# Kernel tuning notes

Hardware: AMD Instinct MI355X
Metric: run time of the kernel (lower is better)

The kernel has to match this reference:

```python
import jax, jax.numpy as jnp
import numpy as np

B, S, H = 32, 1024, 512  # batch, src_len, hidden_dim


def setup_inputs() -> dict:
    key = jax.random.key(0)
    k1, k2, k3, k4, k5 = jax.random.split(key, 5)
    hidden = jax.random.normal(k1, (B, H), dtype=jnp.float32)
    encoder_outputs = jax.random.normal(k2, (B, S, 2 * H), dtype=jnp.float32)
    # nn.Linear(3H, H): weight stored here as [3H, H] (input-major) with bias [H]
    W = jax.random.normal(k3, (3 * H, H), dtype=jnp.float32) / np.sqrt(3 * H)
    b = jax.random.normal(k4, (H,), dtype=jnp.float32) * 0.01
    v = jax.random.normal(k5, (H,), dtype=jnp.float32) / np.sqrt(H)
    return {"hidden": hidden, "encoder_outputs": encoder_outputs, "W": W, "b": b, "v": v}


def reference(hidden, encoder_outputs, W, b, v):
    # concat((repeat(hidden), encoder_outputs)) @ W  ==  hidden @ W[:H] (broadcast) + enc @ W[H:]
    Wh, We = W[:H], W[H:]                         # [H,H], [2H,H]
    h_proj = hidden @ Wh                           # [B,H]
    e_proj = jnp.einsum('bse,eh->bsh', encoder_outputs, We)  # [B,S,H]
    energy = jnp.tanh(h_proj[:, None, :] + e_proj + b)       # [B,S,H]
    # bmm(v[B,1,H], energy^T[B,H,S]) -> scores [B,S]
    scores = jnp.einsum('bsh,h->bs', energy, v)
    return jax.nn.softmax(scores, axis=1)
```

## Files before the change

kernel.cpp:

```cpp
#include <hip/hip_runtime.h>
#include <math.h>

#define B_ 32
#define S_ 1024
#define H_ 512
#define K_ 1024
#define M_ (B_ * S_)

typedef __attribute__((ext_vector_type(8))) short bf16x8;
typedef __attribute__((ext_vector_type(16))) float f32x16;

__device__ __forceinline__ void split_bf16(float f, unsigned short& hi, unsigned short& lo) {
    unsigned u = __float_as_uint(f);
    unsigned r = u + 0x8000u;
    hi = (unsigned short)(r >> 16);
    float fh = __uint_as_float(r & 0xffff0000u);
    float res = f - fh;
    lo = (unsigned short)((__float_as_uint(res) + 0x8000u) >> 16);
}

__device__ __forceinline__ void split8_store(const float4& x, const float4& y,
                                             unsigned short* hiP, unsigned short* loP) {
    float f[8] = {x.x, x.y, x.z, x.w, y.x, y.y, y.z, y.w};
    unsigned hr[8], lr[8];
    #pragma unroll
    for (int i = 0; i < 8; ++i) {
        unsigned u = __float_as_uint(f[i]);
        unsigned r = u + 0x8000u;
        hr[i] = r;
        float fh = __uint_as_float(r & 0xffff0000u);
        lr[i] = __float_as_uint(f[i] - fh) + 0x8000u;
    }
    uint4 Hv, Lv;
    Hv.x = __builtin_amdgcn_perm(hr[1], hr[0], 0x07060302u);
    Hv.y = __builtin_amdgcn_perm(hr[3], hr[2], 0x07060302u);
    Hv.z = __builtin_amdgcn_perm(hr[5], hr[4], 0x07060302u);
    Hv.w = __builtin_amdgcn_perm(hr[7], hr[6], 0x07060302u);
    Lv.x = __builtin_amdgcn_perm(lr[1], lr[0], 0x07060302u);
    Lv.y = __builtin_amdgcn_perm(lr[3], lr[2], 0x07060302u);
    Lv.z = __builtin_amdgcn_perm(lr[5], lr[4], 0x07060302u);
    Lv.w = __builtin_amdgcn_perm(lr[7], lr[6], 0x07060302u);
    *reinterpret_cast<uint4*>(hiP) = Hv;
    *reinterpret_cast<uint4*>(loP) = Lv;
}

__device__ __forceinline__ float fast_tanh(float x) {
    float xc = fminf(fmaxf(x, -15.f), 15.f);
    float t = __expf(2.0f * xc);
    return (t - 1.0f) * __builtin_amdgcn_rcpf(t + 1.0f);
}

__device__ __forceinline__ void async_copy16(const void* g, void* l) {
    __builtin_amdgcn_global_load_lds(
        (const __attribute__((address_space(1))) void*)g,
        (__attribute__((address_space(3))) void*)l, 16, 0, 0);
}

__global__ __launch_bounds__(256) void prep_kernel(
    const float* __restrict__ hidden, const float* __restrict__ W,
    const float* __restrict__ bias, float* __restrict__ hb,
    unsigned short* __restrict__ Wh, unsigned short* __restrict__ Wl)
{
    __shared__ float red[4][64];
    __shared__ float t[32][33];
    const int bx = blockIdx.x;
    if (bx < 256) {
        const int tid = threadIdx.x;
        const int h0  = (bx & 7) * 64;
        const int b   = bx >> 3;
        const int h   = h0 + (tid & 63);
        const int ks  = tid >> 6;
        const float* hrow = hidden + b * H_;
        float acc = 0.f;
        #pragma unroll 8
        for (int k = ks * 128; k < ks * 128 + 128; ++k)
            acc = fmaf(hrow[k], W[(size_t)k * H_ + h], acc);
        red[ks][tid & 63] = acc;
        __syncthreads();
        if (tid < 64)
            hb[b * H_ + h0 + tid] = red[0][tid] + red[1][tid] + red[2][tid]
                                  + red[3][tid] + bias[h0 + tid];
    } else {
        const float* We = W + (size_t)H_ * H_;
        const int cx = bx - 256;
        const int k0 = (cx & 31) * 32, n0 = (cx >> 5) * 32;
        const int tx = threadIdx.x & 31, ty = threadIdx.x >> 5;
        #pragma unroll
        for (int j = 0; j < 4; ++j) {
            const int k = ty + 8 * j;
            t[k][tx] = We[(size_t)(k0 + k) * H_ + n0 + tx];
        }
        __syncthreads();
        #pragma unroll
        for (int j = 0; j < 4; ++j) {
            const int n = ty + 8 * j;
            unsigned short hi, lo;
            split_bf16(t[tx][n], hi, lo);
            Wh[(size_t)(n0 + n) * K_ + k0 + tx] = hi;
            Wl[(size_t)(n0 + n) * K_ + k0 + tx] = lo;
        }
    }
}

__global__ __launch_bounds__(256, 2) void gemm_fused(
    const float* __restrict__ EO,
    const unsigned short* __restrict__ Bth,
    const unsigned short* __restrict__ Btl,
    const float* __restrict__ hb, const float* __restrict__ v,
    float* __restrict__ partial)
{
    __shared__ unsigned short ldsA[2][2][4096];
    __shared__ unsigned short ldsB[2][2][4096];

    const int tid  = threadIdx.x;
    const int bid  = blockIdx.x;
    const int j    = bid >> 3;
    const int mt   = (bid & 7) * 32 + (j >> 2);
    const int nt   = j & 3;
    const int row0 = mt * 128;
    const int col0 = nt * 128;
    const int batch = row0 >> 10;

    const int lane   = tid & 63;
    const int wave   = tid >> 6;
    const int wm     = wave >> 1, wn = wave & 1;
    const int lane32 = lane & 31, khalf = lane >> 5;

    size_t gaA[2];
    int offA[2];
    #pragma unroll
    for (int s = 0; s < 2; ++s) {
        const int seg = tid + 256 * s;
        const int m = seg >> 2, sg = seg & 3;
        gaA[s] = (size_t)(row0 + m) * K_ + sg * 8;
        offA[s] = m * 32 + (sg ^ ((m >> 1) & 3)) * 8;
    }
    size_t gb[2];
    int offB[2];
    #pragma unroll
    for (int jj = 0; jj < 2; ++jj) {
        const int iss = wave * 2 + jj;
        const int r   = iss * 16 + (lane >> 2);
        const int qg  = (lane & 3) ^ ((r >> 1) & 3);
        gb[jj] = (size_t)(col0 + r) * K_ + qg * 8;
        offB[jj] = iss * 512;
    }

    f32x16 acc[2][2];
    #pragma unroll
    for (int fi = 0; fi < 2; ++fi)
        #pragma unroll
        for (int fj = 0; fj < 2; ++fj)
            #pragma unroll
            for (int e = 0; e < 16; ++e)
                acc[fi][fj][e] = 0.f;

    float4 a0[2], a1[2];
    #pragma unroll
    for (int s = 0; s < 2; ++s) {
        a0[s] = *reinterpret_cast<const float4*>(EO + gaA[s]);
        a1[s] = *reinterpret_cast<const float4*>(EO + gaA[s] + 4);
    }
    #pragma unroll
    for (int jj = 0; jj < 2; ++jj) {
        async_copy16(Bth + gb[jj], &ldsB[0][0][offB[jj]]);
        async_copy16(Btl + gb[jj], &ldsB[0][1][offB[jj]]);
    }
    #pragma unroll
    for (int s = 0; s < 2; ++s)
        split8_store(a0[s], a1[s], &ldsA[0][0][offA[s]], &ldsA[0][1][offA[s]]);

    for (int i = 0; i < 32; ++i) {
        __syncthreads();
        const int cur = i & 1, nxt = cur ^ 1;
        const int k0n = 32 * (i + 1);
        if (i < 31) {
            #pragma unroll
            for (int s = 0; s < 2; ++s) {
                a0[s] = *reinterpret_cast<const float4*>(EO + gaA[s] + k0n);
                a1[s] = *reinterpret_cast<const float4*>(EO + gaA[s] + k0n + 4);
            }
            #pragma unroll
            for (int jj = 0; jj < 2; ++jj) {
                async_copy16(Bth + gb[jj] + k0n, &ldsB[nxt][0][offB[jj]]);
                async_copy16(Btl + gb[jj] + k0n, &ldsB[nxt][1][offB[jj]]);
            }
        }

        bf16x8 a_h[2][2], a_l[2][2], b_h[2][2], b_l[2][2];
        #pragma unroll
        for (int fi = 0; fi < 2; ++fi) {
            const int m   = wm * 64 + fi * 32 + lane32;
            const int swz = (m >> 1) & 3;
            #pragma unroll
            for (int ks = 0; ks < 2; ++ks) {
                const int sa = (ks * 2 + khalf) ^ swz;
                a_h[fi][ks] = *reinterpret_cast<const bf16x8*>(&ldsA[cur][0][m * 32 + sa * 8]);
                a_l[fi][ks] = *reinterpret_cast<const bf16x8*>(&ldsA[cur][1][m * 32 + sa * 8]);
            }
        }
        #pragma unroll
        for (int fj = 0; fj < 2; ++fj) {
            const int n   = wn * 64 + fj * 32 + lane32;
            const int swz = (n >> 1) & 3;
            #pragma unroll
            for (int ks = 0; ks < 2; ++ks) {
                const int sb = (ks * 2 + khalf) ^ swz;
                b_h[fj][ks] = *reinterpret_cast<const bf16x8*>(&ldsB[cur][0][n * 32 + sb * 8]);
                b_l[fj][ks] = *reinterpret_cast<const bf16x8*>(&ldsB[cur][1][n * 32 + sb * 8]);
            }
        }
        #pragma unroll
        for (int fi = 0; fi < 2; ++fi)
            #pragma unroll
            for (int fj = 0; fj < 2; ++fj)
                #pragma unroll
                for (int ks = 0; ks < 2; ++ks) {
                    acc[fi][fj] = __builtin_amdgcn_mfma_f32_32x32x16_bf16(
                        a_h[fi][ks], b_h[fj][ks], acc[fi][fj], 0, 0, 0);
                    acc[fi][fj] = __builtin_amdgcn_mfma_f32_32x32x16_bf16(
                        a_h[fi][ks], b_l[fj][ks], acc[fi][fj], 0, 0, 0);
                    acc[fi][fj] = __builtin_amdgcn_mfma_f32_32x32x16_bf16(
                        a_l[fi][ks], b_h[fj][ks], acc[fi][fj], 0, 0, 0);
                }

        if (i < 31) {
            #pragma unroll
            for (int s = 0; s < 2; ++s)
                split8_store(a0[s], a1[s],
                             &ldsA[nxt][0][offA[s]], &ldsA[nxt][1][offA[s]]);
        }
    }

    const float* hb_row = hb + batch * H_;
    float hbv[2], vv[2];
    #pragma unroll
    for (int fj = 0; fj < 2; ++fj) {
        const int c = col0 + wn * 64 + fj * 32 + lane32;
        hbv[fj] = hb_row[c];
        vv[fj]  = v[c];
    }
    float* red = reinterpret_cast<float*>(&ldsA[0][0][0]);
    #pragma unroll
    for (int fi = 0; fi < 2; ++fi)
        #pragma unroll
        for (int r = 0; r < 16; ++r) {
            float rs = 0.f;
            #pragma unroll
            for (int fj = 0; fj < 2; ++fj)
                rs = fmaf(fast_tanh(acc[fi][fj][r] + hbv[fj]), vv[fj], rs);
            rs += __shfl_xor(rs, 1, 64);
            rs += __shfl_xor(rs, 2, 64);
            rs += __shfl_xor(rs, 4, 64);
            rs += __shfl_xor(rs, 8, 64);
            rs += __shfl_xor(rs, 16, 64);
            if (lane32 == 0) {
                const int row = wm * 64 + fi * 32 + (r & 3) + 8 * (r >> 2) + 4 * khalf;
                red[row * 2 + wn] = rs;
            }
        }
    __syncthreads();
    if (tid < 128)
        partial[(size_t)nt * M_ + row0 + tid] = red[tid * 2] + red[tid * 2 + 1];
}

__global__ __launch_bounds__(256) void softmax_kernel(
    const float* __restrict__ partial, float* __restrict__ out)
{
    const int b = blockIdx.x;
    const int tid = threadIdx.x;
    float val[4];
    float lmax = -3.0e38f;
    #pragma unroll
    for (int q = 0; q < 4; ++q) {
        const int idx = b * S_ + tid + 256 * q;
        float sum = partial[idx] + partial[M_ + idx] + partial[2 * M_ + idx] +
                    partial[3 * M_ + idx];
        val[q] = sum;
        lmax = fmaxf(lmax, sum);
    }
    #pragma unroll
    for (int off = 32; off > 0; off >>= 1)
        lmax = fmaxf(lmax, __shfl_down(lmax, off, 64));
    __shared__ float wmax[4];
    if ((tid & 63) == 0) wmax[tid >> 6] = lmax;
    __syncthreads();
    const float gmax = fmaxf(fmaxf(wmax[0], wmax[1]), fmaxf(wmax[2], wmax[3]));
    float lsum = 0.0f;
    #pragma unroll
    for (int q = 0; q < 4; ++q) {
        val[q] = expf(val[q] - gmax);
        lsum += val[q];
    }
    #pragma unroll
    for (int off = 32; off > 0; off >>= 1)
        lsum += __shfl_down(lsum, off, 64);
    __shared__ float wsum[4];
    if ((tid & 63) == 0) wsum[tid >> 6] = lsum;
    __syncthreads();
    const float inv = 1.0f / (wsum[0] + wsum[1] + wsum[2] + wsum[3]);
    #pragma unroll
    for (int q = 0; q < 4; ++q)
        out[b * S_ + tid + 256 * q] = val[q] * inv;
}

extern "C" void kernel_launch(void* const* d_in, const int* in_sizes, int n_in,
                              void* d_out, int out_size, void* d_ws, size_t ws_size,
                              hipStream_t stream) {
    const float* hidden = (const float*)d_in[0];
    const float* EO     = (const float*)d_in[1];
    const float* W      = (const float*)d_in[2];
    const float* bias   = (const float*)d_in[3];
    const float* v      = (const float*)d_in[4];
    float* out          = (float*)d_out;

    float* hb      = (float*)d_ws;
    float* partial = hb + B_ * H_;
    unsigned short* Wth = (unsigned short*)(partial + 4 * M_);
    unsigned short* Wtl = Wth + (size_t)H_ * K_;

    prep_kernel<<<768, 256, 0, stream>>>(hidden, W, bias, hb, Wth, Wtl);
    gemm_fused<<<dim3(1024), 256, 0, stream>>>(EO, Wth, Wtl, hb, v, partial);
    softmax_kernel<<<B_, 256, 0, stream>>>(partial, out);
}
```

Baseline: 320.2 us.

## Load GEMM fragments directly from global memory, bypassing LDS staging

```diff
diff --git a/kernel.cpp b/kernel.cpp
--- a/kernel.cpp
+++ b/kernel.cpp
@@ -19,8 +19,8 @@
     lo = (unsigned short)((__float_as_uint(res) + 0x8000u) >> 16);
 }
 
-__device__ __forceinline__ void split8_store(const float4& x, const float4& y,
-                                             unsigned short* hiP, unsigned short* loP) {
+__device__ __forceinline__ void split8_frag(const float4& x, const float4& y,
+                                            bf16x8& hi, bf16x8& lo) {
     float f[8] = {x.x, x.y, x.z, x.w, y.x, y.y, y.z, y.w};
     unsigned hr[8], lr[8];
     #pragma unroll
@@ -31,29 +31,23 @@
         float fh = __uint_as_float(r & 0xffff0000u);
         lr[i] = __float_as_uint(f[i] - fh) + 0x8000u;
     }
-    uint4 Hv, Lv;
-    Hv.x = __builtin_amdgcn_perm(hr[1], hr[0], 0x07060302u);
-    Hv.y = __builtin_amdgcn_perm(hr[3], hr[2], 0x07060302u);
-    Hv.z = __builtin_amdgcn_perm(hr[5], hr[4], 0x07060302u);
-    Hv.w = __builtin_amdgcn_perm(hr[7], hr[6], 0x07060302u);
-    Lv.x = __builtin_amdgcn_perm(lr[1], lr[0], 0x07060302u);
-    Lv.y = __builtin_amdgcn_perm(lr[3], lr[2], 0x07060302u);
-    Lv.z = __builtin_amdgcn_perm(lr[5], lr[4], 0x07060302u);
-    Lv.w = __builtin_amdgcn_perm(lr[7], lr[6], 0x07060302u);
-    *reinterpret_cast<uint4*>(hiP) = Hv;
-    *reinterpret_cast<uint4*>(loP) = Lv;
+    union { uint4 u; bf16x8 v; } H, L;
+    H.u.x = __builtin_amdgcn_perm(hr[1], hr[0], 0x07060302u);
+    H.u.y = __builtin_amdgcn_perm(hr[3], hr[2], 0x07060302u);
+    H.u.z = __builtin_amdgcn_perm(hr[5], hr[4], 0x07060302u);
+    H.u.w = __builtin_amdgcn_perm(hr[7], hr[6], 0x07060302u);
+    L.u.x = __builtin_amdgcn_perm(lr[1], lr[0], 0x07060302u);
+    L.u.y = __builtin_amdgcn_perm(lr[3], lr[2], 0x07060302u);
+    L.u.z = __builtin_amdgcn_perm(lr[5], lr[4], 0x07060302u);
+    L.u.w = __builtin_amdgcn_perm(lr[7], lr[6], 0x07060302u);
+    hi = H.v;
+    lo = L.v;
 }
 
 __device__ __forceinline__ float fast_tanh(float x) {
     float xc = fminf(fmaxf(x, -15.f), 15.f);
     float t = __expf(2.0f * xc);
     return (t - 1.0f) * __builtin_amdgcn_rcpf(t + 1.0f);
-}
-
-__device__ __forceinline__ void async_copy16(const void* g, void* l) {
-    __builtin_amdgcn_global_load_lds(
-        (const __attribute__((address_space(1))) void*)g,
-        (__attribute__((address_space(3))) void*)l, 16, 0, 0);
 }
 
 __global__ __launch_bounds__(256) void prep_kernel(
@@ -93,11 +87,17 @@
         __syncthreads();
         #pragma unroll
         for (int j = 0; j < 4; ++j) {
-            const int n = ty + 8 * j;
+            const int n    = ty + 8 * j;
+            const int ncol = n0 + n;
+            const int k    = k0 + tx;
             unsigned short hi, lo;
             split_bf16(t[tx][n], hi, lo);
-            Wh[(size_t)(n0 + n) * K_ + k0 + tx] = hi;
-            Wl[(size_t)(n0 + n) * K_ + k0 + tx] = lo;
+            const int c     = ncol >> 5;
+            const int tt    = k >> 4;
+            const int lane_ = ((k >> 3) & 1) * 32 + (ncol & 31);
+            const size_t s  = ((size_t)(c * 64 + tt) * 64 + lane_) * 8 + (k & 7);
+            Wh[s] = hi;
+            Wl[s] = lo;
         }
     }
 }
@@ -109,14 +109,13 @@
     const float* __restrict__ hb, const float* __restrict__ v,
     float* __restrict__ partial)
 {
-    __shared__ unsigned short ldsA[2][2][4096];
-    __shared__ unsigned short ldsB[2][2][4096];
+    __shared__ float red[256];
 
     const int tid  = threadIdx.x;
     const int bid  = blockIdx.x;
-    const int j    = bid >> 3;
-    const int mt   = (bid & 7) * 32 + (j >> 2);
-    const int nt   = j & 3;
+    const int jb   = bid >> 3;
+    const int mt   = (bid & 7) * 32 + (jb >> 2);
+    const int nt   = jb & 3;
     const int row0 = mt * 128;
     const int col0 = nt * 128;
     const int batch = row0 >> 10;
@@ -126,24 +125,18 @@
     const int wm     = wave >> 1, wn = wave & 1;
     const int lane32 = lane & 31, khalf = lane >> 5;
 
-    size_t gaA[2];
-    int offA[2];
-    #pragma unroll
-    for (int s = 0; s < 2; ++s) {
-        const int seg = tid + 256 * s;
-        const int m = seg >> 2, sg = seg & 3;
-        gaA[s] = (size_t)(row0 + m) * K_ + sg * 8;
-        offA[s] = m * 32 + (sg ^ ((m >> 1) & 3)) * 8;
-    }
-    size_t gb[2];
-    int offB[2];
-    #pragma unroll
-    for (int jj = 0; jj < 2; ++jj) {
-        const int iss = wave * 2 + jj;
-        const int r   = iss * 16 + (lane >> 2);
-        const int qg  = (lane & 3) ^ ((r >> 1) & 3);
-        gb[jj] = (size_t)(col0 + r) * K_ + qg * 8;
-        offB[jj] = iss * 512;
+    const float* aP[2];
+    #pragma unroll
+    for (int fi = 0; fi < 2; ++fi)
+        aP[fi] = EO + (size_t)(row0 + wm * 64 + fi * 32 + lane32) * K_ + khalf * 8;
+
+    const unsigned short* bPh[2];
+    const unsigned short* bPl[2];
+    #pragma unroll
+    for (int fj = 0; fj < 2; ++fj) {
+        const int c = nt * 4 + wn * 2 + fj;
+        bPh[fj] = Bth + (size_t)(c * 64) * 512 + lane * 8;
+        bPl[fj] = Btl + (size_t)(c * 64) * 512 + lane * 8;
     }
 
     f32x16 acc[2][2];
@@ -155,82 +148,66 @@
             for (int e = 0; e < 16; ++e)
                 acc[fi][fj][e] = 0.f;
 
-    float4 a0[2], a1[2];
-    #pragma unroll
-    for (int s = 0; s < 2; ++s) {
-        a0[s] = *reinterpret_cast<const float4*>(EO + gaA[s]);
-        a1[s] = *reinterpret_cast<const float4*>(EO + gaA[s] + 4);
-    }
-    #pragma unroll
-    for (int jj = 0; jj < 2; ++jj) {
-        async_copy16(Bth + gb[jj], &ldsB[0][0][offB[jj]]);
-        async_copy16(Btl + gb[jj], &ldsB[0][1][offB[jj]]);
-    }
-    #pragma unroll
-    for (int s = 0; s < 2; ++s)
-        split8_store(a0[s], a1[s], &ldsA[0][0][offA[s]], &ldsA[0][1][offA[s]]);
-
-    for (int i = 0; i < 32; ++i) {
-        __syncthreads();
-        const int cur = i & 1, nxt = cur ^ 1;
-        const int k0n = 32 * (i + 1);
-        if (i < 31) {
-            #pragma unroll
-            for (int s = 0; s < 2; ++s) {
-                a0[s] = *reinterpret_cast<const float4*>(EO + gaA[s] + k0n);
-                a1[s] = *reinterpret_cast<const float4*>(EO + gaA[s] + k0n + 4);
-            }
-            #pragma unroll
-            for (int jj = 0; jj < 2; ++jj) {
-                async_copy16(Bth + gb[jj] + k0n, &ldsB[nxt][0][offB[jj]]);
-                async_copy16(Btl + gb[jj] + k0n, &ldsB[nxt][1][offB[jj]]);
-            }
-        }
-
-        bf16x8 a_h[2][2], a_l[2][2], b_h[2][2], b_l[2][2];
-        #pragma unroll
-        for (int fi = 0; fi < 2; ++fi) {
-            const int m   = wm * 64 + fi * 32 + lane32;
-            const int swz = (m >> 1) & 3;
-            #pragma unroll
-            for (int ks = 0; ks < 2; ++ks) {
-                const int sa = (ks * 2 + khalf) ^ swz;
-                a_h[fi][ks] = *reinterpret_cast<const bf16x8*>(&ldsA[cur][0][m * 32 + sa * 8]);
-                a_l[fi][ks] = *reinterpret_cast<const bf16x8*>(&ldsA[cur][1][m * 32 + sa * 8]);
-            }
-        }
-        #pragma unroll
-        for (int fj = 0; fj < 2; ++fj) {
-            const int n   = wn * 64 + fj * 32 + lane32;
-            const int swz = (n >> 1) & 3;
-            #pragma unroll
-            for (int ks = 0; ks < 2; ++ks) {
-                const int sb = (ks * 2 + khalf) ^ swz;
-                b_h[fj][ks] = *reinterpret_cast<const bf16x8*>(&ldsB[cur][0][n * 32 + sb * 8]);
-                b_l[fj][ks] = *reinterpret_cast<const bf16x8*>(&ldsB[cur][1][n * 32 + sb * 8]);
-            }
-        }
-        #pragma unroll
-        for (int fi = 0; fi < 2; ++fi)
-            #pragma unroll
-            for (int fj = 0; fj < 2; ++fj)
-                #pragma unroll
-                for (int ks = 0; ks < 2; ++ks) {
-                    acc[fi][fj] = __builtin_amdgcn_mfma_f32_32x32x16_bf16(
-                        a_h[fi][ks], b_h[fj][ks], acc[fi][fj], 0, 0, 0);
-                    acc[fi][fj] = __builtin_amdgcn_mfma_f32_32x32x16_bf16(
-                        a_h[fi][ks], b_l[fj][ks], acc[fi][fj], 0, 0, 0);
-                    acc[fi][fj] = __builtin_amdgcn_mfma_f32_32x32x16_bf16(
-                        a_l[fi][ks], b_h[fj][ks], acc[fi][fj], 0, 0, 0);
-                }
-
-        if (i < 31) {
-            #pragma unroll
-            for (int s = 0; s < 2; ++s)
-                split8_store(a0[s], a1[s],
-                             &ldsA[nxt][0][offA[s]], &ldsA[nxt][1][offA[s]]);
-        }
-    }
+    float4 Afp[2][2][2];
+    bf16x8 Bh0[2][2], Bl0[2][2], Bh1[2][2], Bl1[2][2];
+    #pragma unroll
+    for (int fi = 0; fi < 2; ++fi)
+        #pragma unroll
+        for (int ks = 0; ks < 2; ++ks) {
+            Afp[fi][ks][0] = *reinterpret_cast<const float4*>(aP[fi] + ks * 16);
+            Afp[fi][ks][1] = *reinterpret_cast<const float4*>(aP[fi] + ks * 16 + 4);
+        }
+    #pragma unroll
+    for (int fj = 0; fj < 2; ++fj)
+        #pragma unroll
+        for (int ks = 0; ks < 2; ++ks) {
+            Bh0[fj][ks] = *reinterpret_cast<const bf16x8*>(bPh[fj] + ks * 512);
+            Bl0[fj][ks] = *reinterpret_cast<const bf16x8*>(bPl[fj] + ks * 512);
+        }
+
+#define STEP(BHc, BLc, BHn, BLn, I, PF)                                        \
+  {                                                                            \
+    if (PF) {                                                                  \
+      _Pragma("unroll") for (int fj = 0; fj < 2; ++fj)                         \
+        _Pragma("unroll") for (int ks = 0; ks < 2; ++ks) {                     \
+          BHn[fj][ks] = *reinterpret_cast<const bf16x8*>(                      \
+              bPh[fj] + ((I) + 1) * 1024 + ks * 512);                          \
+          BLn[fj][ks] = *reinterpret_cast<const bf16x8*>(                      \
+              bPl[fj] + ((I) + 1) * 1024 + ks * 512);                          \
+        }                                                                      \
+    }                                                                          \
+    bf16x8 ah[2][2], al[2][2];                                                 \
+    _Pragma("unroll") for (int fi = 0; fi < 2; ++fi)                           \
+      _Pragma("unroll") for (int ks = 0; ks < 2; ++ks)                         \
+        split8_frag(Afp[fi][ks][0], Afp[fi][ks][1], ah[fi][ks], al[fi][ks]);   \
+    if (PF) {                                                                  \
+      _Pragma("unroll") for (int fi = 0; fi < 2; ++fi)                         \
+        _Pragma("unroll") for (int ks = 0; ks < 2; ++ks) {                     \
+          Afp[fi][ks][0] = *reinterpret_cast<const float4*>(                   \
+              aP[fi] + ((I) + 1) * 32 + ks * 16);                              \
+          Afp[fi][ks][1] = *reinterpret_cast<const float4*>(                   \
+              aP[fi] + ((I) + 1) * 32 + ks * 16 + 4);                          \
+        }                                                                      \
+    }                                                                          \
+    _Pragma("unroll") for (int fi = 0; fi < 2; ++fi)                           \
+      _Pragma("unroll") for (int fj = 0; fj < 2; ++fj)                         \
+        _Pragma("unroll") for (int ks = 0; ks < 2; ++ks) {                     \
+          acc[fi][fj] = __builtin_amdgcn_mfma_f32_32x32x16_bf16(               \
+              ah[fi][ks], BHc[fj][ks], acc[fi][fj], 0, 0, 0);                  \
+          acc[fi][fj] = __builtin_amdgcn_mfma_f32_32x32x16_bf16(               \
+              ah[fi][ks], BLc[fj][ks], acc[fi][fj], 0, 0, 0);                  \
+          acc[fi][fj] = __builtin_amdgcn_mfma_f32_32x32x16_bf16(               \
+              al[fi][ks], BHc[fj][ks], acc[fi][fj], 0, 0, 0);                  \
+        }                                                                      \
+  }
+
+    for (int it = 0; it < 15; ++it) {
+        STEP(Bh0, Bl0, Bh1, Bl1, 2 * it,     1);
+        STEP(Bh1, Bl1, Bh0, Bl0, 2 * it + 1, 1);
+    }
+    STEP(Bh0, Bl0, Bh1, Bl1, 30, 1);
+    STEP(Bh1, Bl1, Bh0, Bl0, 31, 0);
+#undef STEP
 
     const float* hb_row = hb + batch * H_;
     float hbv[2], vv[2];
@@ -240,7 +217,6 @@
         hbv[fj] = hb_row[c];
         vv[fj]  = v[c];
     }
-    float* red = reinterpret_cast<float*>(&ldsA[0][0][0]);
     #pragma unroll
     for (int fi = 0; fi < 2; ++fi)
         #pragma unroll
```

After: 350.9 us. 1.1x slower.

## Enlarge GEMM tile to 256x256 with 512 threads and pre-swizzled weight layout

Applied to the files above, without the earlier changes.

```diff
diff --git a/kernel.cpp b/kernel.cpp
--- a/kernel.cpp
+++ b/kernel.cpp
@@ -93,62 +93,62 @@
         __syncthreads();
         #pragma unroll
         for (int j = 0; j < 4; ++j) {
-            const int n = ty + 8 * j;
+            const int n    = ty + 8 * j;
+            const int ncol = n0 + n;
+            const int k    = k0 + tx;
             unsigned short hi, lo;
             split_bf16(t[tx][n], hi, lo);
-            Wh[(size_t)(n0 + n) * K_ + k0 + tx] = hi;
-            Wl[(size_t)(n0 + n) * K_ + k0 + tx] = lo;
-        }
-    }
-}
-
-__global__ __launch_bounds__(256, 2) void gemm_fused(
+            const int c     = ncol >> 5;
+            const int tt    = k >> 4;
+            const int lane_ = ((k >> 3) & 1) * 32 + (ncol & 31);
+            const size_t s  = ((size_t)(c * 64 + tt) * 64 + lane_) * 8 + (k & 7);
+            Wh[s] = hi;
+            Wl[s] = lo;
+        }
+    }
+}
+
+__global__ __launch_bounds__(512, 2) void gemm_fused(
     const float* __restrict__ EO,
     const unsigned short* __restrict__ Bth,
     const unsigned short* __restrict__ Btl,
     const float* __restrict__ hb, const float* __restrict__ v,
     float* __restrict__ partial)
 {
-    __shared__ unsigned short ldsA[2][2][4096];
-    __shared__ unsigned short ldsB[2][2][4096];
+    __shared__ unsigned short ldsA[2][2][8192];
+    __shared__ unsigned short ldsB[2][2][8192];
 
     const int tid  = threadIdx.x;
     const int bid  = blockIdx.x;
-    const int j    = bid >> 3;
-    const int mt   = (bid & 7) * 32 + (j >> 2);
-    const int nt   = j & 3;
-    const int row0 = mt * 128;
-    const int col0 = nt * 128;
+    const int jb   = bid >> 3;
+    const int mt   = (bid & 7) * 16 + (jb >> 1);
+    const int nt   = jb & 1;
+    const int row0 = mt * 256;
+    const int col0 = nt * 256;
     const int batch = row0 >> 10;
 
     const int lane   = tid & 63;
     const int wave   = tid >> 6;
-    const int wm     = wave >> 1, wn = wave & 1;
-    const int lane32 = lane & 31, khalf = lane >> 5;
-
-    size_t gaA[2];
-    int offA[2];
+    const int wm     = wave >> 2, wn = wave & 3;
+    const int lane32 = lane & 31, kh = lane >> 5;
+
+    size_t gA[2];
+    int offAw[2];
     #pragma unroll
     for (int s = 0; s < 2; ++s) {
-        const int seg = tid + 256 * s;
+        const int seg = tid + 512 * s;
         const int m = seg >> 2, sg = seg & 3;
-        gaA[s] = (size_t)(row0 + m) * K_ + sg * 8;
-        offA[s] = m * 32 + (sg ^ ((m >> 1) & 3)) * 8;
-    }
-    size_t gb[2];
-    int offB[2];
-    #pragma unroll
-    for (int jj = 0; jj < 2; ++jj) {
-        const int iss = wave * 2 + jj;
-        const int r   = iss * 16 + (lane >> 2);
-        const int qg  = (lane & 3) ^ ((r >> 1) & 3);
-        gb[jj] = (size_t)(col0 + r) * K_ + qg * 8;
-        offB[jj] = iss * 512;
-    }
-
-    f32x16 acc[2][2];
-    #pragma unroll
-    for (int fi = 0; fi < 2; ++fi)
+        gA[s]    = (size_t)(row0 + m) * K_ + sg * 8;
+        offAw[s] = ((m >> 5) * 2 + (sg >> 1)) * 512
+                 + ((sg & 1) * 32 + ((m & 31) ^ sg)) * 8;
+    }
+    const unsigned short* gBh = Bth + ((size_t)(nt * 8 + wave) * 32768 + lane * 8);
+    const unsigned short* gBl = Btl + ((size_t)(nt * 8 + wave) * 32768 + lane * 8);
+    const int offBw = wave * 1024;
+
+    f32x16 acc[4][2];
+    #pragma unroll
+    for (int fi = 0; fi < 4; ++fi)
         #pragma unroll
         for (int fj = 0; fj < 2; ++fj)
             #pragma unroll
@@ -158,77 +158,73 @@
     float4 a0[2], a1[2];
     #pragma unroll
     for (int s = 0; s < 2; ++s) {
-        a0[s] = *reinterpret_cast<const float4*>(EO + gaA[s]);
-        a1[s] = *reinterpret_cast<const float4*>(EO + gaA[s] + 4);
-    }
-    #pragma unroll
-    for (int jj = 0; jj < 2; ++jj) {
-        async_copy16(Bth + gb[jj], &ldsB[0][0][offB[jj]]);
-        async_copy16(Btl + gb[jj], &ldsB[0][1][offB[jj]]);
+        a0[s] = *reinterpret_cast<const float4*>(EO + gA[s]);
+        a1[s] = *reinterpret_cast<const float4*>(EO + gA[s] + 4);
+    }
+    #pragma unroll
+    for (int ks = 0; ks < 2; ++ks) {
+        async_copy16(gBh + ks * 512, &ldsB[0][0][offBw + ks * 512]);
+        async_copy16(gBl + ks * 512, &ldsB[0][1][offBw + ks * 512]);
     }
     #pragma unroll
     for (int s = 0; s < 2; ++s)
-        split8_store(a0[s], a1[s], &ldsA[0][0][offA[s]], &ldsA[0][1][offA[s]]);
+        split8_store(a0[s], a1[s], &ldsA[0][0][offAw[s]], &ldsA[0][1][offAw[s]]);
 
     for (int i = 0; i < 32; ++i) {
         __syncthreads();
         const int cur = i & 1, nxt = cur ^ 1;
-        const int k0n = 32 * (i + 1);
         if (i < 31) {
+            const int k0n = 32 * (i + 1);
             #pragma unroll
             for (int s = 0; s < 2; ++s) {
-                a0[s] = *reinterpret_cast<const float4*>(EO + gaA[s] + k0n);
-                a1[s] = *reinterpret_cast<const float4*>(EO + gaA[s] + k0n + 4);
-            }
-            #pragma unroll
-            for (int jj = 0; jj < 2; ++jj) {
-                async_copy16(Bth + gb[jj] + k0n, &ldsB[nxt][0][offB[jj]]);
-                async_copy16(Btl + gb[jj] + k0n, &ldsB[nxt][1][offB[jj]]);
-            }
-        }
-
-        bf16x8 a_h[2][2], a_l[2][2], b_h[2][2], b_l[2][2];
-        #pragma unroll
-        for (int fi = 0; fi < 2; ++fi) {
-            const int m   = wm * 64 + fi * 32 + lane32;
-            const int swz = (m >> 1) & 3;
+                a0[s] = *reinterpret_cast<const float4*>(EO + gA[s] + k0n);
+                a1[s] = *reinterpret_cast<const float4*>(EO + gA[s] + k0n + 4);
+            }
+            const int tnxt = 2 * (i + 1);
             #pragma unroll
             for (int ks = 0; ks < 2; ++ks) {
-                const int sa = (ks * 2 + khalf) ^ swz;
-                a_h[fi][ks] = *reinterpret_cast<const bf16x8*>(&ldsA[cur][0][m * 32 + sa * 8]);
-                a_l[fi][ks] = *reinterpret_cast<const bf16x8*>(&ldsA[cur][1][m * 32 + sa * 8]);
-            }
-        }
-        #pragma unroll
-        for (int fj = 0; fj < 2; ++fj) {
-            const int n   = wn * 64 + fj * 32 + lane32;
-            const int swz = (n >> 1) & 3;
+                async_copy16(gBh + (tnxt + ks) * 512, &ldsB[nxt][0][offBw + ks * 512]);
+                async_copy16(gBl + (tnxt + ks) * 512, &ldsB[nxt][1][offBw + ks * 512]);
+            }
+        }
+
+        bf16x8 b_h[2][2], b_l[2][2];
+        #pragma unroll
+        for (int fj = 0; fj < 2; ++fj)
             #pragma unroll
             for (int ks = 0; ks < 2; ++ks) {
-                const int sb = (ks * 2 + khalf) ^ swz;
-                b_h[fj][ks] = *reinterpret_cast<const bf16x8*>(&ldsB[cur][0][n * 32 + sb * 8]);
-                b_l[fj][ks] = *reinterpret_cast<const bf16x8*>(&ldsB[cur][1][n * 32 + sb * 8]);
-            }
-        }
-        #pragma unroll
-        for (int fi = 0; fi < 2; ++fi)
+                const int baseB = ((wn * 2 + fj) * 2 + ks) * 512 + lane * 8;
+                b_h[fj][ks] = *reinterpret_cast<const bf16x8*>(&ldsB[cur][0][baseB]);
+                b_l[fj][ks] = *reinterpret_cast<const bf16x8*>(&ldsB[cur][1][baseB]);
+            }
+        #pragma unroll
+        for (int fi = 0; fi < 4; ++fi) {
+            bf16x8 a_h[2], a_l[2];
+            #pragma unroll
+            for (int ks = 0; ks < 2; ++ks) {
+                const int baseA = ((wm * 4 + fi) * 2 + ks) * 512
+                                + (kh * 32 + (lane32 ^ (2 * ks + kh))) * 8;
+                a_h[ks] = *reinterpret_cast<const bf16x8*>(&ldsA[cur][0][baseA]);
+                a_l[ks] = *reinterpret_cast<const bf16x8*>(&ldsA[cur][1][baseA]);
+            }
             #pragma unroll
             for (int fj = 0; fj < 2; ++fj)
                 #pragma unroll
                 for (int ks = 0; ks < 2; ++ks) {
                     acc[fi][fj] = __builtin_amdgcn_mfma_f32_32x32x16_bf16(
-                        a_h[fi][ks], b_h[fj][ks], acc[fi][fj], 0, 0, 0);
+                        a_h[ks], b_h[fj][ks], acc[fi][fj], 0, 0, 0);
                     acc[fi][fj] = __builtin_amdgcn_mfma_f32_32x32x16_bf16(
-                        a_h[fi][ks], b_l[fj][ks], acc[fi][fj], 0, 0, 0);
+                        a_h[ks], b_l[fj][ks], acc[fi][fj], 0, 0, 0);
                     acc[fi][fj] = __builtin_amdgcn_mfma_f32_32x32x16_bf16(
-                        a_l[fi][ks], b_h[fj][ks], acc[fi][fj], 0, 0, 0);
+                        a_l[ks], b_h[fj][ks], acc[fi][fj], 0, 0, 0);
                 }
+        }
 
         if (i < 31) {
             #pragma unroll
             for (int s = 0; s < 2; ++s)
                 split8_store(a0[s], a1[s],
-                             &ldsA[nxt][0][offA[s]], &ldsA[nxt][1][offA[s]]);
+                             &ldsA[nxt][0][offAw[s]], &ldsA[nxt][1][offAw[s]]);
         }
     }
 
@@ -236,13 +232,13 @@
     float hbv[2], vv[2];
     #pragma unroll
     for (int fj = 0; fj < 2; ++fj) {
-        const int c = col0 + wn * 64 + fj * 32 + lane32;
+        const int c = col0 + (wn * 2 + fj) * 32 + lane32;
         hbv[fj] = hb_row[c];
         vv[fj]  = v[c];
     }
     float* red = reinterpret_cast<float*>(&ldsA[0][0][0]);
     #pragma unroll
-    for (int fi = 0; fi < 2; ++fi)
+    for (int fi = 0; fi < 4; ++fi)
         #pragma unroll
         for (int r = 0; r < 16; ++r) {
             float rs = 0.f;
@@ -255,13 +251,14 @@
             rs += __shfl_xor(rs, 8, 64);
             rs += __shfl_xor(rs, 16, 64);
             if (lane32 == 0) {
-                const int row = wm * 64 + fi * 32 + (r & 3) + 8 * (r >> 2) + 4 * khalf;
-                red[row * 2 + wn] = rs;
+                const int row = wm * 128 + fi * 32 + (r & 3) + 8 * (r >> 2) + 4 * kh;
+                red[row * 4 + wn] = rs;
             }
         }
     __syncthreads();
-    if (tid < 128)
-        partial[(size_t)nt * M_ + row0 + tid] = red[tid * 2] + red[tid * 2 + 1];
+    if (tid < 256)
+        partial[(size_t)nt * M_ + row0 + tid] =
+            red[tid * 4] + red[tid * 4 + 1] + red[tid * 4 + 2] + red[tid * 4 + 3];
 }
 
 __global__ __launch_bounds__(256) void softmax_kernel(
@@ -274,8 +271,7 @@
     #pragma unroll
     for (int q = 0; q < 4; ++q) {
         const int idx = b * S_ + tid + 256 * q;
-        float sum = partial[idx] + partial[M_ + idx] + partial[2 * M_ + idx] +
-                    partial[3 * M_ + idx];
+        float sum = partial[idx] + partial[M_ + idx];
         val[q] = sum;
         lmax = fmaxf(lmax, sum);
     }
@@ -320,6 +316,6 @@
     unsigned short* Wtl = Wth + (size_t)H_ * K_;
 
     prep_kernel<<<768, 256, 0, stream>>>(hidden, W, bias, hb, Wth, Wtl);
-    gemm_fused<<<dim3(1024), 256, 0, stream>>>(EO, Wth, Wtl, hb, v, partial);
+    gemm_fused<<<dim3(256), 512, 0, stream>>>(EO, Wth, Wtl, hb, v, partial);
     softmax_kernel<<<B_, 256, 0, stream>>>(partial, out);
 }
```

Result: faster. 287.7 us (-10.1%).
